# Optimization experiments

Measured on AMD Instinct MI355X. Metric: run time of the kernel, lower is better.

The kernel has to match this reference:

```python
import jax, jax.numpy as jnp
import numpy as np

H = 2048; FF = 8192; NH = 16; HD = 128; R = 16; SCALING = 2.0  # alpha/r = 32/16
EPS = 1e-5
NLEV = 15.0  # 2**4 - 1 levels for 4-bit quantization

def _quantize(key, out_f, in_f):
    # mirrors QuantizedLinear.quantize_weights on a randn*0.02 init weight
    w = jax.random.normal(key, (out_f, in_f), dtype=jnp.float32) * 0.02
    wmin = w.min(axis=1, keepdims=True)
    wmax = w.max(axis=1, keepdims=True)
    rng = jnp.clip(wmax - wmin, 1e-6)
    sc = rng / NLEV
    q = jnp.clip(jnp.round((w - wmin) / sc), 0, NLEV).astype(jnp.int8)
    return q, sc[:, 0], wmin[:, 0]

def setup_inputs():
    key = jax.random.key(0)
    ks = jax.random.split(key, 22)
    dims = [('q', H, H), ('k', H, H), ('v', H, H), ('o', H, H), ('g', FF, H), ('u', FF, H), ('d', H, FF)]
    d = {}
    i = 0
    for name, of, inf in dims:
        qw, sc, zp = _quantize(ks[i], of, inf); i += 1
        d[name + '_qw'] = qw; d[name + '_sc'] = sc; d[name + '_zp'] = zp
        d[name + '_A'] = jax.random.normal(ks[i], (R, inf), dtype=jnp.float32) * 0.01; i += 1
        d[name + '_B'] = jax.random.normal(ks[i], (of, R), dtype=jnp.float32) * 0.01; i += 1
    d['x'] = jax.random.normal(ks[i], (2, 2048, H), dtype=jnp.float32)
    d['ln1_w'] = jnp.ones(H); d['ln1_b'] = jnp.zeros(H)
    d['ln2_w'] = jnp.ones(H); d['ln2_b'] = jnp.zeros(H)
    return d

def _forward(x, qws, ps, lns):
    def lin(h, i):
        sc, zp, A, B = ps[i]
        # dequantize int8 weight (per-row scale/zero-point) + LoRA low-rank update
        W = qws[i].astype(jnp.float32) * sc[:, None] + zp[:, None] + (B @ A) * SCALING
        return h @ W.T
    def ln(h, w, b):
        mu = h.mean(-1, keepdims=True)
        var = h.var(-1, keepdims=True)  # biased, matches torch LayerNorm
        return (h - mu) / jnp.sqrt(var + EPS) * w + b
    ln1_w, ln1_b, ln2_w, ln2_b = lns
    Bsz, S, _ = x.shape
    h = ln(x, ln1_w, ln1_b)
    q = lin(h, 0).reshape(Bsz, S, NH, HD)
    k = lin(h, 1).reshape(Bsz, S, NH, HD)
    v = lin(h, 2).reshape(Bsz, S, NH, HD)
    attn = jnp.einsum('bqhd,bkhd->bhqk', q, k) / (HD ** 0.5)
    attn = jax.nn.softmax(attn, axis=-1)  # dropout is identity in eval
    o = jnp.einsum('bhqk,bkhd->bqhd', attn, v).reshape(Bsz, S, H)
    x1 = x + lin(o, 3)
    h2 = ln(x1, ln2_w, ln2_b)
    ff = jax.nn.silu(lin(h2, 4)) * lin(h2, 5)
    return x1 + lin(ff, 6)

def reference(x, q_qw, q_sc, q_zp, q_A, q_B, k_qw, k_sc, k_zp, k_A, k_B, v_qw, v_sc, v_zp, v_A, v_B, o_qw, o_sc, o_zp, o_A, o_B, g_qw, g_sc, g_zp, g_A, g_B, u_qw, u_sc, u_zp, u_A, u_B, d_qw, d_sc, d_zp, d_A, d_B, ln1_w, ln1_b, ln2_w, ln2_b):
    qws = (q_qw, k_qw, v_qw, o_qw, g_qw, u_qw, d_qw)
    ps = [(q_sc, q_zp, q_A, q_B), (k_sc, k_zp, k_A, k_B), (v_sc, v_zp, v_A, v_B), (o_sc, o_zp, o_A, o_B), (g_sc, g_zp, g_A, g_B), (u_sc, u_zp, u_A, u_B), (d_sc, d_zp, d_A, d_B)]
    return _forward(x, qws, ps, (ln1_w, ln1_b, ln2_w, ln2_b))
```

## Files before the change

### kernel.cpp

```cpp
#include <hip/hip_runtime.h>
#include <cstdint>
#include <cstddef>

#define GLOBAL_AS __attribute__((address_space(1)))
#define LDS_AS    __attribute__((address_space(3)))

typedef __bf16 bf16;
typedef __bf16 bf16x4 __attribute__((ext_vector_type(4)));
typedef __bf16 bf16x8 __attribute__((ext_vector_type(8)));
typedef float  f32x4  __attribute__((ext_vector_type(4)));
typedef int    i32x4  __attribute__((ext_vector_type(4)));
typedef unsigned int u32x2 __attribute__((ext_vector_type(2)));

__device__ __forceinline__ void gl_lds16(const void* g, void* l) {
  __builtin_amdgcn_global_load_lds((GLOBAL_AS void*)g, (LDS_AS void*)l, 16, 0, 0);
}

__global__ __launch_bounds__(256) void ln_kernel(const float* __restrict__ x,
                                                 const float* __restrict__ w,
                                                 const float* __restrict__ bias,
                                                 bf16* __restrict__ out) {
  const int row = blockIdx.x;
  const int tid = threadIdx.x;
  const float* xr = x + (size_t)row * 2048;
  f32x4 v0 = ((const f32x4*)xr)[tid * 2];
  f32x4 v1 = ((const f32x4*)xr)[tid * 2 + 1];
  float s = 0.f, ss = 0.f;
#pragma unroll
  for (int j = 0; j < 4; ++j) { s += v0[j]; ss += v0[j] * v0[j]; }
#pragma unroll
  for (int j = 0; j < 4; ++j) { s += v1[j]; ss += v1[j] * v1[j]; }
#pragma unroll
  for (int d = 1; d < 64; d <<= 1) { s += __shfl_xor(s, d); ss += __shfl_xor(ss, d); }
  __shared__ float red[8];
  const int wave = tid >> 6, lane = tid & 63;
  if (lane == 0) { red[wave * 2] = s; red[wave * 2 + 1] = ss; }
  __syncthreads();
  s  = red[0] + red[2] + red[4] + red[6];
  ss = red[1] + red[3] + red[5] + red[7];
  const float mean = s * (1.f / 2048.f);
  const float var  = ss * (1.f / 2048.f) - mean * mean;
  const float rstd = rsqrtf(var + 1e-5f);
  const int col = tid * 8;
  bf16x8 o;
#pragma unroll
  for (int j = 0; j < 4; ++j) o[j]     = (bf16)((v0[j] - mean) * rstd * w[col + j]     + bias[col + j]);
#pragma unroll
  for (int j = 0; j < 4; ++j) o[4 + j] = (bf16)((v1[j] - mean) * rstd * w[col + 4 + j] + bias[col + 4 + j]);
  *(bf16x8*)(out + (size_t)row * 2048 + col) = o;
}

__global__ __launch_bounds__(256) void ln_q_kernel(const float* __restrict__ x,
    const float* __restrict__ w, const float* __restrict__ bias,
    char* __restrict__ qh, float* __restrict__ s_m, float* __restrict__ rs,
    float* __restrict__ de) {
  const int row = blockIdx.x;
  const int tid = threadIdx.x;
  const float* xr = x + (size_t)row * 2048;
  f32x4 v0 = ((const f32x4*)xr)[tid * 2];
  f32x4 v1 = ((const f32x4*)xr)[tid * 2 + 1];
  float s = 0.f, ss = 0.f;
#pragma unroll
  for (int j = 0; j < 4; ++j) { s += v0[j]; ss += v0[j] * v0[j]; }
#pragma unroll
  for (int j = 0; j < 4; ++j) { s += v1[j]; ss += v1[j] * v1[j]; }
#pragma unroll
  for (int d = 1; d < 64; d <<= 1) { s += __shfl_xor(s, d); ss += __shfl_xor(ss, d); }
  __shared__ float red[12];
  const int wave = tid >> 6, lane = tid & 63;
  if (lane == 0) { red[wave * 2] = s; red[wave * 2 + 1] = ss; }
  __syncthreads();
  s  = red[0] + red[2] + red[4] + red[6];
  ss = red[1] + red[3] + red[5] + red[7];
  const float mean = s * (1.f / 2048.f);
  const float var  = ss * (1.f / 2048.f) - mean * mean;
  const float rstd = rsqrtf(var + 1e-5f);
  const int col = tid * 8;
  float y[8];
#pragma unroll
  for (int j = 0; j < 4; ++j) y[j]     = (v0[j] - mean) * rstd * w[col + j]     + bias[col + j];
#pragma unroll
  for (int j = 0; j < 4; ++j) y[4 + j] = (v1[j] - mean) * rstd * w[col + 4 + j] + bias[col + 4 + j];
  float sy = 0.f, mx = 0.f;
#pragma unroll
  for (int j = 0; j < 8; ++j) { sy += y[j]; mx = fmaxf(mx, fabsf(y[j])); }
#pragma unroll
  for (int d = 1; d < 64; d <<= 1) { sy += __shfl_xor(sy, d); mx = fmaxf(mx, __shfl_xor(mx, d)); }
  __syncthreads();
  if (lane == 0) { red[wave * 2] = sy; red[wave * 2 + 1] = mx; }
  __syncthreads();
  const float sya = red[0] + red[2] + red[4] + red[6];
  const float mxa = fmaxf(fmaxf(red[1], red[3]), fmaxf(red[5], red[7]));
  const float inv = 127.f / fmaxf(mxa, 1e-8f);
  unsigned int lo = 0, hi = 0;
  int qs = 0;
#pragma unroll
  for (int j = 0; j < 4; ++j) { int qi = (int)rintf(y[j] * inv);     qs += qi; lo |= ((unsigned int)qi & 0xffu) << (8 * j); }
#pragma unroll
  for (int j = 0; j < 4; ++j) { int qi = (int)rintf(y[4 + j] * inv); qs += qi; hi |= ((unsigned int)qi & 0xffu) << (8 * j); }
  u32x2 st; st[0] = lo; st[1] = hi;
  *(u32x2*)(qh + (size_t)row * 2048 + col) = st;
  float fqs = (float)qs;
#pragma unroll
  for (int d = 1; d < 64; d <<= 1) fqs += __shfl_xor(fqs, d);
  __syncthreads();
  if (lane == 0) red[8 + wave] = fqs;
  __syncthreads();
  if (tid == 0) {
    const float qsa = red[8] + red[9] + red[10] + red[11];
    const float smv = fmaxf(mxa, 1e-8f) / 127.f;
    s_m[row] = smv; rs[row] = sya; de[row] = sya - smv * qsa;
  }
}

__global__ __launch_bounds__(256) void dequant_kernel(const int* __restrict__ qw,
    const float* __restrict__ sc, const float* __restrict__ zp,
    const float* __restrict__ A, const float* __restrict__ Bm,
    bf16* __restrict__ W, int out_f, int in_f) {
  const int per_row = in_f >> 3;
  const int idx = blockIdx.x * 256 + threadIdx.x;
  const int o  = idx / per_row;
  const int i0 = (idx - o * per_row) << 3;
  const float s = sc[o], z = zp[o];
  float bl[16];
#pragma unroll
  for (int r = 0; r < 16; ++r) bl[r] = Bm[o * 16 + r];
  float acc[8] = {0.f, 0.f, 0.f, 0.f, 0.f, 0.f, 0.f, 0.f};
#pragma unroll
  for (int r = 0; r < 16; ++r) {
    const f32x4* ap = (const f32x4*)(A + (size_t)r * in_f + i0);
    f32x4 a0 = ap[0], a1 = ap[1];
#pragma unroll
    for (int j = 0; j < 4; ++j) { acc[j] += bl[r] * a0[j]; acc[4 + j] += bl[r] * a1[j]; }
  }
  const int* qp = qw + (size_t)o * in_f + i0;
  bf16x8 w8;
#pragma unroll
  for (int j = 0; j < 8; ++j) w8[j] = (bf16)((float)qp[j] * s + z + 2.f * acc[j]);
  *(bf16x8*)(W + (size_t)o * in_f + i0) = w8;
}

__global__ __launch_bounds__(256) void pack_w_kernel(const int* __restrict__ qw,
    const float* __restrict__ sc, char* __restrict__ out, float* __restrict__ wsum) {
  const int row = blockIdx.x;
  const int tid = threadIdx.x;
  const size_t idx = (size_t)row * 2048 + tid * 8;
  i32x4 a = *(const i32x4*)(qw + idx);
  i32x4 b = *(const i32x4*)(qw + idx + 4);
  unsigned int lo = ((unsigned)a[0] & 0xffu) | (((unsigned)a[1] & 0xffu) << 8) |
                    (((unsigned)a[2] & 0xffu) << 16) | (((unsigned)a[3] & 0xffu) << 24);
  unsigned int hi = ((unsigned)b[0] & 0xffu) | (((unsigned)b[1] & 0xffu) << 8) |
                    (((unsigned)b[2] & 0xffu) << 16) | (((unsigned)b[3] & 0xffu) << 24);
  u32x2 st; st[0] = lo; st[1] = hi;
  *(u32x2*)(out + idx) = st;
  float fs = (float)(a[0] + a[1] + a[2] + a[3] + b[0] + b[1] + b[2] + b[3]);
#pragma unroll
  for (int d = 1; d < 64; d <<= 1) fs += __shfl_xor(fs, d);
  __shared__ float red[4];
  const int wave = tid >> 6, lane = tid & 63;
  if (lane == 0) red[wave] = fs;
  __syncthreads();
  if (tid == 0) wsum[row] = sc[row] * (red[0] + red[1] + red[2] + red[3]) * (1.f / 2048.f);
}

__global__ __launch_bounds__(256) void pack_b2_kernel(const float* __restrict__ gB,
    const float* __restrict__ uB, bf16* __restrict__ B2g, bf16* __restrict__ B2u) {
  const int idx = blockIdx.x * 256 + threadIdx.x;
  const int nn = idx >> 5, r = idx & 31;
  B2g[idx] = (r < 16)  ? (bf16)(2.f * gB[nn * 16 + r])        : (bf16)0.f;
  B2u[idx] = (r >= 16) ? (bf16)(2.f * uB[nn * 16 + (r - 16)]) : (bf16)0.f;
}

__global__ __launch_bounds__(256) void hA_kernel(const char* __restrict__ qh,
    const float* __restrict__ s_m, const float* __restrict__ Ag,
    const float* __restrict__ Au, bf16* __restrict__ hA) {
  __shared__ bf16 Asm[32 * 512];
  const int tid = threadIdx.x, wave = tid >> 6, lane = tid & 63;
  const int row = blockIdx.x * 4 + wave;
  float acc[32];
#pragma unroll
  for (int r = 0; r < 32; ++r) acc[r] = 0.f;
  for (int kb = 0; kb < 2048; kb += 512) {
    const int r2 = tid >> 3, c0 = (tid & 7) * 64;
    const float* src = (r2 < 16 ? Ag + (size_t)r2 * 2048 : Au + (size_t)(r2 - 16) * 2048) + kb + c0;
#pragma unroll
    for (int j = 0; j < 64; j += 8) {
      f32x4 va = *(const f32x4*)(src + j);
      f32x4 vb = *(const f32x4*)(src + j + 4);
      bf16x8 bv;
#pragma unroll
      for (int jj = 0; jj < 4; ++jj) { bv[jj] = (bf16)va[jj]; bv[4 + jj] = (bf16)vb[jj]; }
      *(bf16x8*)(Asm + r2 * 512 + c0 + j) = bv;
    }
    __syncthreads();
    float q[8];
    const char* qp = qh + (size_t)row * 2048 + kb + lane * 8;
#pragma unroll
    for (int j = 0; j < 8; ++j) q[j] = (float)qp[j];
#pragma unroll
    for (int r = 0; r < 32; ++r) {
      bf16x8 a8 = *(const bf16x8*)(Asm + r * 512 + lane * 8);
      float d = 0.f;
#pragma unroll
      for (int j = 0; j < 8; ++j) d += q[j] * (float)a8[j];
      acc[r] += d;
    }
    __syncthreads();
  }
  const float s = s_m[row];
#pragma unroll
  for (int r = 0; r < 32; ++r) {
    float v = acc[r];
#pragma unroll
    for (int d = 1; d < 64; d <<= 1) v += __shfl_xor(v, d);
    if (lane == 0) hA[(size_t)row * 32 + r] = (bf16)(s * v);
  }
}

#define STAGE_A(t, buf, r8) gl_lds16(Ag + (size_t)(r8) * 8 * K + (size_t)(t) * 64, \
                                     &As[buf][((wave * 32) + (r8) * 8) * 64])
#define STAGE_B(t, buf, r8) gl_lds16(Bg + (size_t)(r8) * 8 * K + (size_t)(t) * 64, \
                                     &Bs[buf][((wave * 16) + (r8) * 8) * 64])

template <int MODE>
__global__ __launch_bounds__(512, 2) void gemm8_kernel(const bf16* __restrict__ A,
    const bf16* __restrict__ B, bf16* __restrict__ Cb, float* __restrict__ Cf,
    const float* __restrict__ res, bf16* __restrict__ vt,
    int M, int N, int K, int ldc) {
  const int tid = threadIdx.x;
  const int wave = tid >> 6, lane = tid & 63;
  const int lcol = lane & 15, lrow = lane >> 4;
  const int wm = (wave >> 1) * 64, wn = (wave & 1) * 64;
  const int nwg = gridDim.x * gridDim.y;
  const int bid = blockIdx.y * gridDim.x + blockIdx.x;
  const int swb = (bid & 7) * (nwg >> 3) + (bid >> 3);
  const int n0 = (swb % gridDim.x) * 128;
  const int m0 = (swb / gridDim.x) * 256;
  __shared__ bf16 As[3][256 * 64];
  __shared__ bf16 Bs[3][128 * 64];
  f32x4 acc[4][4] = {};
  const int sw = ((lane & 7) ^ ((lane >> 3) & 7)) * 8;
  const bf16* Ag = A + (size_t)(m0 + wave * 32 + (lane >> 3)) * K + sw;
  const bf16* Bg = B + (size_t)(n0 + wave * 16 + (lane >> 3)) * K + sw;
  const int nt = K >> 6;

#pragma unroll
  for (int r8 = 0; r8 < 4; ++r8) STAGE_A(0, 0, r8);
  STAGE_B(0, 0, 0); STAGE_B(0, 0, 1);
#pragma unroll
  for (int r8 = 0; r8 < 4; ++r8) STAGE_A(1, 1, r8);
  STAGE_B(1, 1, 0); STAGE_B(1, 1, 1);
  asm volatile("s_waitcnt vmcnt(6)" ::: "memory");
  __builtin_amdgcn_s_barrier();

  int cur = 0;
  for (int t = 0; t < nt; ++t) {
    const bf16* Ac = As[cur];
    const bf16* Bc = Bs[cur];
    const int nx = (cur >= 1) ? cur - 1 : 2;
    const bool pf = (t + 2 < nt);

    bf16x8 a0[4], b0[4];
#pragma unroll
    for (int j = 0; j < 4; ++j)
      b0[j] = *(const bf16x8*)(Bc + (wn + j * 16 + lcol) * 64 + (lrow ^ (lcol & 7)) * 8);
#pragma unroll
    for (int i = 0; i < 4; ++i)
      a0[i] = *(const bf16x8*)(Ac + (wm + i * 16 + lcol) * 64 + (lrow ^ (lcol & 7)) * 8);
    if (pf) { STAGE_A(t + 2, nx, 0); STAGE_A(t + 2, nx, 1); STAGE_B(t + 2, nx, 0); }
    __builtin_amdgcn_s_barrier();
    __builtin_amdgcn_s_setprio(1);
#pragma unroll
    for (int i = 0; i < 4; ++i)
#pragma unroll
      for (int j = 0; j < 4; ++j)
        acc[i][j] = __builtin_amdgcn_mfma_f32_16x16x32_bf16(a0[i], b0[j], acc[i][j], 0, 0, 0);
    __builtin_amdgcn_s_setprio(0);
    __builtin_amdgcn_s_barrier();

    bf16x8 a1[4], b1[4];
#pragma unroll
    for (int j = 0; j < 4; ++j)
      b1[j] = *(const bf16x8*)(Bc + (wn + j * 16 + lcol) * 64 + ((4 + lrow) ^ (lcol & 7)) * 8);
#pragma unroll
    for (int i = 0; i < 4; ++i)
      a1[i] = *(const bf16x8*)(Ac + (wm + i * 16 + lcol) * 64 + ((4 + lrow) ^ (lcol & 7)) * 8);
    if (pf) { STAGE_A(t + 2, nx, 2); STAGE_A(t + 2, nx, 3); STAGE_B(t + 2, nx, 1); }
    __builtin_amdgcn_s_barrier();
    __builtin_amdgcn_s_setprio(1);
#pragma unroll
    for (int i = 0; i < 4; ++i)
#pragma unroll
      for (int j = 0; j < 4; ++j)
        acc[i][j] = __builtin_amdgcn_mfma_f32_16x16x32_bf16(a1[i], b1[j], acc[i][j], 0, 0, 0);
    __builtin_amdgcn_s_setprio(0);
    if (pf) asm volatile("s_waitcnt vmcnt(6)" ::: "memory");
    else    asm volatile("s_waitcnt vmcnt(0)" ::: "memory");
    __builtin_amdgcn_s_barrier();
    cur = (cur == 2) ? 0 : cur + 1;
  }

#pragma unroll
  for (int i = 0; i < 4; ++i)
#pragma unroll
    for (int j = 0; j < 4; ++j) {
      const int row0 = m0 + wm + i * 16 + lrow * 4;
      const int col  = n0 + wn + j * 16 + lcol;
      if (MODE == 3 && col >= 4096) {
        const int c2 = col - 4096;
        bf16x4 v4;
#pragma unroll
        for (int r = 0; r < 4; ++r) v4[r] = (bf16)acc[i][j][r];
        *(bf16x4*)(vt + (size_t)(((row0 >> 11) * 16 + (c2 >> 7)) * 128 + (c2 & 127)) * 2048
                      + (row0 & 2047)) = v4;
      } else {
#pragma unroll
        for (int r = 0; r < 4; ++r) {
          const int row = row0 + r;
          const float v = acc[i][j][r];
          const size_t idx = (size_t)row * ldc + col;
          if (MODE == 1) Cf[idx] = res[idx] + v;
          else           Cb[idx] = (bf16)v;
        }
      }
    }
}
#undef STAGE_A
#undef STAGE_B

#define STAGE_A8(t, buf, r8) gl_lds16(Ag + (size_t)(r8) * 8 * K + (size_t)(t) * 128, \
                                      &As[buf][((wave * 32) + (r8) * 8) * 128])
#define STAGE_B8(t, buf, r8) gl_lds16(Bg + (size_t)(r8) * 8 * K + (size_t)(t) * 128, \
                                      &Bs[buf][((wave * 16) + (r8) * 8) * 128])

template <int MODE>
__global__ __launch_bounds__(512, 2) void gemm_i8_kernel(const char* __restrict__ Aq,
    const char* __restrict__ Bq, const float* __restrict__ s_m, const float* __restrict__ rs,
    const float* __restrict__ de, const float* __restrict__ sc, const float* __restrict__ zp,
    const float* __restrict__ wsum, const bf16* __restrict__ hA, const bf16* __restrict__ B2,
    bf16* __restrict__ Cb, const bf16* __restrict__ gate, int M, int N, int K) {
  const int tid = threadIdx.x;
  const int wave = tid >> 6, lane = tid & 63;
  const int lcol = lane & 15, lrow = lane >> 4;
  const int wm = (wave >> 1) * 64, wn = (wave & 1) * 64;
  const int nwg = gridDim.x * gridDim.y;
  const int bid = blockIdx.y * gridDim.x + blockIdx.x;
  const int swb = (bid & 7) * (nwg >> 3) + (bid >> 3);
  const int n0 = (swb % gridDim.x) * 128;
  const int m0 = (swb / gridDim.x) * 256;
  __shared__ char As[3][256 * 128];
  __shared__ char Bs[3][128 * 128];
  i32x4 acc[4][4] = {};
  const int sw = ((lane & 7) ^ ((lane >> 3) & 7)) * 16;
  const char* Ag = Aq + (size_t)(m0 + wave * 32 + (lane >> 3)) * K + sw;
  const char* Bg = Bq + (size_t)(n0 + wave * 16 + (lane >> 3)) * K + sw;
  const int nt = K >> 7;

#pragma unroll
  for (int r8 = 0; r8 < 4; ++r8) STAGE_A8(0, 0, r8);
  STAGE_B8(0, 0, 0); STAGE_B8(0, 0, 1);
#pragma unroll
  for (int r8 = 0; r8 < 4; ++r8) STAGE_A8(1, 1, r8);
  STAGE_B8(1, 1, 0); STAGE_B8(1, 1, 1);
  asm volatile("s_waitcnt vmcnt(6)" ::: "memory");
  __builtin_amdgcn_s_barrier();

  int cur = 0;
  for (int t = 0; t < nt; ++t) {
    const char* Ac = As[cur];
    const char* Bc = Bs[cur];
    const int nx = (cur >= 1) ? cur - 1 : 2;
    const bool pf = (t + 2 < nt);

    i32x4 af0[4], bf0[4];
#pragma unroll
    for (int j = 0; j < 4; ++j)
      bf0[j] = *(const i32x4*)(Bc + (wn + j * 16 + lcol) * 128 + (lrow ^ (lcol & 7)) * 16);
#pragma unroll
    for (int i = 0; i < 4; ++i)
      af0[i] = *(const i32x4*)(Ac + (wm + i * 16 + lcol) * 128 + (lrow ^ (lcol & 7)) * 16);
    if (pf) { STAGE_A8(t + 2, nx, 0); STAGE_A8(t + 2, nx, 1); STAGE_B8(t + 2, nx, 0); }
    __builtin_amdgcn_s_barrier();
    __builtin_amdgcn_s_setprio(1);
#pragma unroll
    for (int i = 0; i < 4; ++i)
#pragma unroll
      for (int j = 0; j < 4; ++j)
        acc[i][j] = __builtin_amdgcn_mfma_i32_16x16x64_i8(af0[i], bf0[j], acc[i][j], 0, 0, 0);
    __builtin_amdgcn_s_setprio(0);
    __builtin_amdgcn_s_barrier();

    i32x4 af1[4], bf1[4];
#pragma unroll
    for (int j = 0; j < 4; ++j)
      bf1[j] = *(const i32x4*)(Bc + (wn + j * 16 + lcol) * 128 + ((4 + lrow) ^ (lcol & 7)) * 16);
#pragma unroll
    for (int i = 0; i < 4; ++i)
      af1[i] = *(const i32x4*)(Ac + (wm + i * 16 + lcol) * 128 + ((4 + lrow) ^ (lcol & 7)) * 16);
    if (pf) { STAGE_A8(t + 2, nx, 2); STAGE_A8(t + 2, nx, 3); STAGE_B8(t + 2, nx, 1); }
    __builtin_amdgcn_s_barrier();
    __builtin_amdgcn_s_setprio(1);
#pragma unroll
    for (int i = 0; i < 4; ++i)
#pragma unroll
      for (int j = 0; j < 4; ++j)
        acc[i][j] = __builtin_amdgcn_mfma_i32_16x16x64_i8(af1[i], bf1[j], acc[i][j], 0, 0, 0);
    __builtin_amdgcn_s_setprio(0);
    if (pf) asm volatile("s_waitcnt vmcnt(6)" ::: "memory");
    else    asm volatile("s_waitcnt vmcnt(0)" ::: "memory");
    __builtin_amdgcn_s_barrier();
    cur = (cur == 2) ? 0 : cur + 1;
  }

  bf16x8 ha[4], bb[4];
#pragma unroll
  for (int i = 0; i < 4; ++i) ha[i] = *(const bf16x8*)(hA + (size_t)(m0 + wm + i * 16 + lcol) * 32 + lrow * 8);
#pragma unroll
  for (int j = 0; j < 4; ++j) bb[j] = *(const bf16x8*)(B2 + (size_t)(n0 + wn + j * 16 + lcol) * 32 + lrow * 8);
  float scv[4], zpv[4], wsv[4];
#pragma unroll
  for (int j = 0; j < 4; ++j) {
    const int col = n0 + wn + j * 16 + lcol;
    scv[j] = sc[col]; zpv[j] = zp[col]; wsv[j] = wsum[col];
  }
  float smv[4][4], rsv[4][4], dev[4][4];
#pragma unroll
  for (int i = 0; i < 4; ++i)
#pragma unroll
    for (int r = 0; r < 4; ++r) {
      const int row = m0 + wm + i * 16 + lrow * 4 + r;
      smv[i][r] = s_m[row]; rsv[i][r] = rs[row]; dev[i][r] = de[row];
    }
  const f32x4 zero = {0.f, 0.f, 0.f, 0.f};
#pragma unroll
  for (int i = 0; i < 4; ++i)
#pragma unroll
    for (int j = 0; j < 4; ++j) {
      f32x4 L = __builtin_amdgcn_mfma_f32_16x16x32_bf16(ha[i], bb[j], zero, 0, 0, 0);
#pragma unroll
      for (int r = 0; r < 4; ++r) {
        const int row = m0 + wm + i * 16 + lrow * 4 + r;
        const int col = n0 + wn + j * 16 + lcol;
        const float v = scv[j] * smv[i][r] * (float)acc[i][j][r] + zpv[j] * rsv[i][r]
                      + wsv[j] * dev[i][r] + L[r];
        const size_t idx = (size_t)row * N + col;
        if (MODE == 0) Cb[idx] = (bf16)v;
        else {
          const float g = (float)gate[idx];
          Cb[idx] = (bf16)((g / (1.f + __expf(-g))) * v);
        }
      }
    }
}
#undef STAGE_A8
#undef STAGE_B8

__global__ __launch_bounds__(256) void attn_kernel(const bf16* __restrict__ Cqk,
                                                   const bf16* __restrict__ VtG,
                                                   bf16* __restrict__ obuf) {
  const int qt = blockIdx.x, h = blockIdx.y, b = blockIdx.z;
  const int tid = threadIdx.x, wave = tid >> 6, lane = tid & 63;
  const int lcol = lane & 15, lrow = lane >> 4;
  const int base_m = b * 2048 + qt * 128;
  __shared__ bf16 Ks[64 * 128];
  __shared__ bf16 Vt[128 * 64];
  __shared__ bf16 Ps[4][32 * 72];
  bf16* ps = Ps[wave];
  bf16x8 qf[2][4];
#pragma unroll
  for (int i = 0; i < 2; ++i)
#pragma unroll
    for (int dk = 0; dk < 4; ++dk)
      qf[i][dk] = *(const bf16x8*)(Cqk + (size_t)(base_m + wave * 32 + i * 16 + lcol) * 4096
                                   + h * 128 + dk * 32 + lrow * 8);
  f32x4 of[2][8] = {};
  float m_run[2][4], l_run[2][4];
#pragma unroll
  for (int i = 0; i < 2; ++i)
#pragma unroll
    for (int r = 0; r < 4; ++r) { m_run[i][r] = -1e30f; l_run[i][r] = 0.f; }
  const float SCL2 = 0.12751874972f;
  const int vswz = (lane & 7) ^ (lane >> 3);

  for (int kt = 0; kt < 2048; kt += 64) {
#pragma unroll
    for (int r4 = 0; r4 < 4; ++r4) {
      const int s_low = r4 * 4 + lrow;
      gl_lds16(Cqk + (size_t)(b * 2048 + kt + wave * 16 + s_low) * 4096 + 2048 + h * 128
                   + (lcol ^ s_low) * 8,
               Ks + (wave * 16 + r4 * 4) * 128);
    }
#pragma unroll
    for (int r8 = 0; r8 < 4; ++r8)
      gl_lds16(VtG + (size_t)((b * 16 + h) * 128 + wave * 32 + r8 * 8 + (lane >> 3)) * 2048
                   + kt + vswz * 8,
               Vt + (wave * 32 + r8 * 8) * 64);
    __syncthreads();

    f32x4 sacc[2][4] = {};
#pragma unroll
    for (int jb = 0; jb < 4; ++jb) {
      bf16x8 kf[4];
#pragma unroll
      for (int dk = 0; dk < 4; ++dk)
        kf[dk] = *(const bf16x8*)(Ks + (jb * 16 + lcol) * 128 + ((dk * 4 + lrow) ^ lcol) * 8);
#pragma unroll
      for (int i = 0; i < 2; ++i)
#pragma unroll
        for (int dk = 0; dk < 4; ++dk)
          sacc[i][jb] = __builtin_amdgcn_mfma_f32_16x16x32_bf16(qf[i][dk], kf[dk], sacc[i][jb], 0, 0, 0);
    }

#pragma unroll
    for (int i = 0; i < 2; ++i) {
      float z[4][4], mx[4];
#pragma unroll
      for (int jb = 0; jb < 4; ++jb)
#pragma unroll
        for (int r = 0; r < 4; ++r) z[jb][r] = sacc[i][jb][r] * SCL2;
#pragma unroll
      for (int r = 0; r < 4; ++r)
        mx[r] = fmaxf(fmaxf(z[0][r], z[1][r]), fmaxf(z[2][r], z[3][r]));
#pragma unroll
      for (int d = 1; d < 16; d <<= 1)
#pragma unroll
        for (int r = 0; r < 4; ++r) mx[r] = fmaxf(mx[r], __shfl_xor(mx[r], d));
#pragma unroll
      for (int r = 0; r < 4; ++r) {
        const float mn = fmaxf(m_run[i][r], mx[r]);
        const float alpha = __builtin_amdgcn_exp2f(m_run[i][r] - mn);
        m_run[i][r] = mn;
        float srow = 0.f;
#pragma unroll
        for (int jb = 0; jb < 4; ++jb) {
          const float p = __builtin_amdgcn_exp2f(z[jb][r] - mn);
          z[jb][r] = p; srow += p;
        }
        l_run[i][r] = l_run[i][r] * alpha + srow;
#pragma unroll
        for (int db = 0; db < 8; ++db) of[i][db][r] *= alpha;
      }
#pragma unroll
      for (int jb = 0; jb < 4; ++jb)
#pragma unroll
        for (int r = 0; r < 4; ++r)
          ps[(i * 16 + lrow * 4 + r) * 72 + jb * 16 + lcol] = (bf16)z[jb][r];
    }

#pragma unroll
    for (int ss = 0; ss < 2; ++ss) {
      bf16x8 a0 = *(const bf16x8*)(ps + (0 * 16 + lcol) * 72 + ss * 32 + lrow * 8);
      bf16x8 a1 = *(const bf16x8*)(ps + (1 * 16 + lcol) * 72 + ss * 32 + lrow * 8);
#pragma unroll
      for (int db = 0; db < 8; ++db) {
        bf16x8 vf = *(const bf16x8*)(Vt + (db * 16 + lcol) * 64 + ((ss * 4 + lrow) ^ (lcol & 7)) * 8);
        of[0][db] = __builtin_amdgcn_mfma_f32_16x16x32_bf16(a0, vf, of[0][db], 0, 0, 0);
        of[1][db] = __builtin_amdgcn_mfma_f32_16x16x32_bf16(a1, vf, of[1][db], 0, 0, 0);
      }
    }
    __syncthreads();
  }
#pragma unroll
  for (int i = 0; i < 2; ++i)
#pragma unroll
    for (int r = 0; r < 4; ++r) {
      float l = l_run[i][r];
#pragma unroll
      for (int d = 1; d < 16; d <<= 1) l += __shfl_xor(l, d);
      const float inv = 1.f / l;
      const size_t rb = (size_t)(base_m + wave * 32 + i * 16 + lrow * 4 + r) * 2048 + h * 128;
#pragma unroll
      for (int db = 0; db < 8; ++db)
        obuf[rb + db * 16 + lcol] = (bf16)(of[i][db][r] * inv);
    }
}

extern "C" void kernel_launch(void* const* d_in, const int* in_sizes, int n_in,
                              void* d_out, int out_size, void* d_ws, size_t ws_size,
                              hipStream_t stream) {
  (void)in_sizes; (void)n_in; (void)out_size; (void)ws_size;
  const int*   q_qw = (const int*)d_in[0];   const float* q_sc = (const float*)d_in[1];
  const float* q_zp = (const float*)d_in[2]; const float* q_A  = (const float*)d_in[3];
  const float* q_B  = (const float*)d_in[4];
  const int*   k_qw = (const int*)d_in[5];   const float* k_sc = (const float*)d_in[6];
  const float* k_zp = (const float*)d_in[7]; const float* k_A  = (const float*)d_in[8];
  const float* k_B  = (const float*)d_in[9];
  const int*   v_qw = (const int*)d_in[10];  const float* v_sc = (const float*)d_in[11];
  const float* v_zp = (const float*)d_in[12];const float* v_A  = (const float*)d_in[13];
  const float* v_B  = (const float*)d_in[14];
  const int*   o_qw = (const int*)d_in[15];  const float* o_sc = (const float*)d_in[16];
  const float* o_zp = (const float*)d_in[17];const float* o_A  = (const float*)d_in[18];
  const float* o_B  = (const float*)d_in[19];
  const int*   g_qw = (const int*)d_in[20];  const float* g_sc = (const float*)d_in[21];
  const float* g_zp = (const float*)d_in[22];const float* g_A  = (const float*)d_in[23];
  const float* g_B  = (const float*)d_in[24];
  const int*   u_qw = (const int*)d_in[25];  const float* u_sc = (const float*)d_in[26];
  const float* u_zp = (const float*)d_in[27];const float* u_A  = (const float*)d_in[28];
  const float* u_B  = (const float*)d_in[29];
  const int*   d_qw = (const int*)d_in[30];  const float* d_sc = (const float*)d_in[31];
  const float* d_zp = (const float*)d_in[32];const float* d_A  = (const float*)d_in[33];
  const float* d_B  = (const float*)d_in[34];
  const float* x    = (const float*)d_in[35];
  const float* ln1w = (const float*)d_in[36];const float* ln1b = (const float*)d_in[37];
  const float* ln2w = (const float*)d_in[38];const float* ln2b = (const float*)d_in[39];

  char* ws = (char*)d_ws;
  bf16* W = (bf16*)ws;
  char* Wg8 = ws;
  char* Wu8 = ws + (size_t)8192 * 2048;
  char* p2  = ws + (size_t)32 * 1024 * 1024;
  bf16* h   = (bf16*)p2;
  char*  qh  = p2;
  float* s_m = (float*)(p2 + 8 * 1024 * 1024);
  float* rs  = (float*)(p2 + 8 * 1024 * 1024 + 16384);
  float* de  = (float*)(p2 + 8 * 1024 * 1024 + 32768);
  bf16*  hA  = (bf16*)(p2 + 8 * 1024 * 1024 + 49152);
  bf16*  B2g = (bf16*)(p2 + 8 * 1024 * 1024 + 49152 + 262144);
  bf16*  B2u = B2g + (size_t)8192 * 32;
  float* wsg = (float*)((char*)(B2u + (size_t)8192 * 32));
  float* wsu = wsg + 8192;
  bf16* C = (bf16*)(ws + (size_t)48 * 1024 * 1024);
  bf16* Cqk = C;
  bf16* VtG = C + (size_t)4096 * 4096;
  bf16* obuf = VtG + (size_t)2 * 16 * 128 * 2048;
  float* x1  = (float*)d_out;
  float* out = (float*)d_out;

  ln_kernel<<<4096, 256, 0, stream>>>(x, ln1w, ln1b, h);
  dequant_kernel<<<2048, 256, 0, stream>>>(q_qw, q_sc, q_zp, q_A, q_B, W, 2048, 2048);
  dequant_kernel<<<2048, 256, 0, stream>>>(k_qw, k_sc, k_zp, k_A, k_B, W + (size_t)2048 * 2048, 2048, 2048);
  dequant_kernel<<<2048, 256, 0, stream>>>(v_qw, v_sc, v_zp, v_A, v_B, W + (size_t)4096 * 2048, 2048, 2048);
  gemm8_kernel<3><<<dim3(48, 16), 512, 0, stream>>>(h, W, Cqk, nullptr, nullptr, VtG, 4096, 6144, 2048, 4096);
  attn_kernel<<<dim3(16, 16, 2), 256, 0, stream>>>(Cqk, VtG, obuf);
  dequant_kernel<<<2048, 256, 0, stream>>>(o_qw, o_sc, o_zp, o_A, o_B, W, 2048, 2048);
  gemm8_kernel<1><<<dim3(16, 16), 512, 0, stream>>>(obuf, W, nullptr, x1, x, nullptr, 4096, 2048, 2048, 2048);
  ln_q_kernel<<<4096, 256, 0, stream>>>(x1, ln2w, ln2b, qh, s_m, rs, de);
  hA_kernel<<<1024, 256, 0, stream>>>(qh, s_m, g_A, u_A, hA);
  pack_w_kernel<<<8192, 256, 0, stream>>>(g_qw, g_sc, Wg8, wsg);
  pack_w_kernel<<<8192, 256, 0, stream>>>(u_qw, u_sc, Wu8, wsu);
  pack_b2_kernel<<<1024, 256, 0, stream>>>(g_B, u_B, B2g, B2u);
  gemm_i8_kernel<0><<<dim3(64, 16), 512, 0, stream>>>(qh, Wg8, s_m, rs, de, g_sc, g_zp, wsg, hA, B2g, C, nullptr, 4096, 8192, 2048);
  gemm_i8_kernel<1><<<dim3(64, 16), 512, 0, stream>>>(qh, Wu8, s_m, rs, de, u_sc, u_zp, wsu, hA, B2u, C, C, 4096, 8192, 2048);
  dequant_kernel<<<8192, 256, 0, stream>>>(d_qw, d_sc, d_zp, d_A, d_B, W, 2048, 8192);
  gemm8_kernel<1><<<dim3(16, 16), 512, 0, stream>>>(C, W, nullptr, out, x1, nullptr, 4096, 2048, 8192, 2048);
}
```

Measured before the change: 1.127 ms.

## Merge QKV dequant launches, add lazy softmax rescale and MFMA priority hints

Replaces the three separate Q/K/V dequant launches with a single kernel that picks the segment from the block index, saving launch overhead and tail effects. In attention, the running-max update and output rescale are skipped when every lane's new block max stays within a threshold of the running max (FA4-style lazy rescaling). Exponentials are then taken against a stale max, which stays exact after final normalization but can grow values by up to 2^8 before rounding to bf16. s_setprio is raised around the MFMA sections to favour matrix-issuing waves.

New measurement: 1.176 ms. +4.4%, slower.

```diff
diff --git a/kernel.cpp b/kernel.cpp
--- a/kernel.cpp
+++ b/kernel.cpp
@@ -113,31 +113,52 @@
   }
 }
 
+__device__ __forceinline__ void dequant_body(const int* qw, const float* sc,
+    const float* zp, const float* A, const float* Bm, bf16* W, int in_f,
+    int bid, int tid) {
+  const int per_row = in_f >> 3;
+  const int idx = bid * 256 + tid;
+  const int o  = idx / per_row;
+  const int i0 = (idx - o * per_row) << 3;
+  const float s = sc[o], z = zp[o];
+  float bl[16];
+#pragma unroll
+  for (int r = 0; r < 16; ++r) bl[r] = Bm[o * 16 + r];
+  float acc[8] = {0.f, 0.f, 0.f, 0.f, 0.f, 0.f, 0.f, 0.f};
+#pragma unroll
+  for (int r = 0; r < 16; ++r) {
+    const f32x4* ap = (const f32x4*)(A + (size_t)r * in_f + i0);
+    f32x4 a0 = ap[0], a1 = ap[1];
+#pragma unroll
+    for (int j = 0; j < 4; ++j) { acc[j] += bl[r] * a0[j]; acc[4 + j] += bl[r] * a1[j]; }
+  }
+  const int* qp = qw + (size_t)o * in_f + i0;
+  bf16x8 w8;
+#pragma unroll
+  for (int j = 0; j < 8; ++j) w8[j] = (bf16)((float)qp[j] * s + z + 2.f * acc[j]);
+  *(bf16x8*)(W + (size_t)o * in_f + i0) = w8;
+}
+
 __global__ __launch_bounds__(256) void dequant_kernel(const int* __restrict__ qw,
     const float* __restrict__ sc, const float* __restrict__ zp,
     const float* __restrict__ A, const float* __restrict__ Bm,
     bf16* __restrict__ W, int out_f, int in_f) {
-  const int per_row = in_f >> 3;
-  const int idx = blockIdx.x * 256 + threadIdx.x;
-  const int o  = idx / per_row;
-  const int i0 = (idx - o * per_row) << 3;
-  const float s = sc[o], z = zp[o];
-  float bl[16];
-#pragma unroll
-  for (int r = 0; r < 16; ++r) bl[r] = Bm[o * 16 + r];
-  float acc[8] = {0.f, 0.f, 0.f, 0.f, 0.f, 0.f, 0.f, 0.f};
-#pragma unroll
-  for (int r = 0; r < 16; ++r) {
-    const f32x4* ap = (const f32x4*)(A + (size_t)r * in_f + i0);
-    f32x4 a0 = ap[0], a1 = ap[1];
-#pragma unroll
-    for (int j = 0; j < 4; ++j) { acc[j] += bl[r] * a0[j]; acc[4 + j] += bl[r] * a1[j]; }
-  }
-  const int* qp = qw + (size_t)o * in_f + i0;
-  bf16x8 w8;
-#pragma unroll
-  for (int j = 0; j < 8; ++j) w8[j] = (bf16)((float)qp[j] * s + z + 2.f * acc[j]);
-  *(bf16x8*)(W + (size_t)o * in_f + i0) = w8;
+  dequant_body(qw, sc, zp, A, Bm, W, in_f, blockIdx.x, threadIdx.x);
+}
+
+__global__ __launch_bounds__(256) void dequant3_kernel(
+    const int* q_qw, const float* q_sc, const float* q_zp, const float* q_A, const float* q_B,
+    const int* k_qw, const float* k_sc, const float* k_zp, const float* k_A, const float* k_B,
+    const int* v_qw, const float* v_sc, const float* v_zp, const float* v_A, const float* v_B,
+    bf16* W) {
+  const int seg = blockIdx.x >> 11;
+  const int bid = blockIdx.x & 2047;
+  const int* qw = (seg == 0) ? q_qw : (seg == 1) ? k_qw : v_qw;
+  const float* sc = (seg == 0) ? q_sc : (seg == 1) ? k_sc : v_sc;
+  const float* zp = (seg == 0) ? q_zp : (seg == 1) ? k_zp : v_zp;
+  const float* A  = (seg == 0) ? q_A  : (seg == 1) ? k_A  : v_A;
+  const float* Bm = (seg == 0) ? q_B  : (seg == 1) ? k_B  : v_B;
+  dequant_body(qw, sc, zp, A, Bm, W + (size_t)seg * 2048 * 2048, 2048, bid, threadIdx.x);
 }
 
 __global__ __launch_bounds__(256) void pack_w_kernel(const int* __restrict__ qw,
@@ -480,6 +501,7 @@
 #pragma unroll
     for (int r = 0; r < 4; ++r) { m_run[i][r] = -1e30f; l_run[i][r] = 0.f; }
   const float SCL2 = 0.12751874972f;
+  const float THR = 8.f;
   const int vswz = (lane & 7) ^ (lane >> 3);
 
   for (int kt = 0; kt < 2048; kt += 64) {
@@ -498,6 +520,7 @@
     __syncthreads();
 
     f32x4 sacc[2][4] = {};
+    __builtin_amdgcn_s_setprio(1);
 #pragma unroll
     for (int jb = 0; jb < 4; ++jb) {
       bf16x8 kf[4];
@@ -510,6 +533,7 @@
         for (int dk = 0; dk < 4; ++dk)
           sacc[i][jb] = __builtin_amdgcn_mfma_f32_16x16x32_bf16(qf[i][dk], kf[dk], sacc[i][jb], 0, 0, 0);
     }
+    __builtin_amdgcn_s_setprio(0);
 
 #pragma unroll
     for (int i = 0; i < 2; ++i) {
@@ -525,20 +549,36 @@
       for (int d = 1; d < 16; d <<= 1)
 #pragma unroll
         for (int r = 0; r < 4; ++r) mx[r] = fmaxf(mx[r], __shfl_xor(mx[r], d));
-#pragma unroll
-      for (int r = 0; r < 4; ++r) {
-        const float mn = fmaxf(m_run[i][r], mx[r]);
-        const float alpha = __builtin_amdgcn_exp2f(m_run[i][r] - mn);
-        m_run[i][r] = mn;
-        float srow = 0.f;
-#pragma unroll
-        for (int jb = 0; jb < 4; ++jb) {
-          const float p = __builtin_amdgcn_exp2f(z[jb][r] - mn);
-          z[jb][r] = p; srow += p;
+      bool ok = true;
+#pragma unroll
+      for (int r = 0; r < 4; ++r) ok = ok && (mx[r] <= m_run[i][r] + THR);
+      if (__all(ok)) {
+#pragma unroll
+        for (int r = 0; r < 4; ++r) {
+          float srow = 0.f;
+#pragma unroll
+          for (int jb = 0; jb < 4; ++jb) {
+            const float p = __builtin_amdgcn_exp2f(z[jb][r] - m_run[i][r]);
+            z[jb][r] = p; srow += p;
+          }
+          l_run[i][r] += srow;
         }
-        l_run[i][r] = l_run[i][r] * alpha + srow;
-#pragma unroll
-        for (int db = 0; db < 8; ++db) of[i][db][r] *= alpha;
+      } else {
+#pragma unroll
+        for (int r = 0; r < 4; ++r) {
+          const float mn = fmaxf(m_run[i][r], mx[r]);
+          const float alpha = __builtin_amdgcn_exp2f(m_run[i][r] - mn);
+          m_run[i][r] = mn;
+          float srow = 0.f;
+#pragma unroll
+          for (int jb = 0; jb < 4; ++jb) {
+            const float p = __builtin_amdgcn_exp2f(z[jb][r] - mn);
+            z[jb][r] = p; srow += p;
+          }
+          l_run[i][r] = l_run[i][r] * alpha + srow;
+#pragma unroll
+          for (int db = 0; db < 8; ++db) of[i][db][r] *= alpha;
+        }
       }
 #pragma unroll
       for (int jb = 0; jb < 4; ++jb)
@@ -547,6 +587,7 @@
           ps[(i * 16 + lrow * 4 + r) * 72 + jb * 16 + lcol] = (bf16)z[jb][r];
     }
 
+    __builtin_amdgcn_s_setprio(1);
 #pragma unroll
     for (int ss = 0; ss < 2; ++ss) {
       bf16x8 a0 = *(const bf16x8*)(ps + (0 * 16 + lcol) * 72 + ss * 32 + lrow * 8);
@@ -558,6 +599,7 @@
         of[1][db] = __builtin_amdgcn_mfma_f32_16x16x32_bf16(a1, vf, of[1][db], 0, 0, 0);
       }
     }
+    __builtin_amdgcn_s_setprio(0);
     __syncthreads();
   }
 #pragma unroll
@@ -627,9 +669,9 @@
   float* out = (float*)d_out;
 
   ln_kernel<<<4096, 256, 0, stream>>>(x, ln1w, ln1b, h);
-  dequant_kernel<<<2048, 256, 0, stream>>>(q_qw, q_sc, q_zp, q_A, q_B, W, 2048, 2048);
-  dequant_kernel<<<2048, 256, 0, stream>>>(k_qw, k_sc, k_zp, k_A, k_B, W + (size_t)2048 * 2048, 2048, 2048);
-  dequant_kernel<<<2048, 256, 0, stream>>>(v_qw, v_sc, v_zp, v_A, v_B, W + (size_t)4096 * 2048, 2048, 2048);
+  dequant3_kernel<<<6144, 256, 0, stream>>>(q_qw, q_sc, q_zp, q_A, q_B,
+                                            k_qw, k_sc, k_zp, k_A, k_B,
+                                            v_qw, v_sc, v_zp, v_A, v_B, W);
   gemm8_kernel<3><<<dim3(48, 16), 512, 0, stream>>>(h, W, Cqk, nullptr, nullptr, VtG, 4096, 6144, 2048, 4096);
   attn_kernel<<<dim3(16, 16, 2), 256, 0, stream>>>(Cqk, VtG, obuf);
   dequant_kernel<<<2048, 256, 0, stream>>>(o_qw, o_sc, o_zp, o_A, o_B, W, 2048, 2048);
```
